# Optimization experiments

Measured on AMD Instinct MI355X. Metric: run time of the kernel, lower is better.

## Reference

```python
import jax, jax.numpy as jnp
import numpy as np
import math

D = 256          # cubic grid size
THICKNESS = 20   # sponge thickness
DT = 0.001
N_PML = 2
R_PML = 0.001


def _build_sigma(vmax, shape, thickness):
    # vectorized equivalent of the torch slab-assignment loop:
    # final value at a point is damping(min distance to any face) if < thickness else 0
    sigma0 = -(N_PML + 1) * vmax * math.log(R_PML) / (2.0 * thickness)
    dists = []
    for ax, n in enumerate(shape):
        idx = jnp.arange(n)
        d = jnp.minimum(idx, n - 1 - idx)
        sh = [1, 1, 1]
        sh[ax] = n
        dists.append(d.reshape(sh))
    mind = jnp.minimum(jnp.minimum(
        jnp.broadcast_to(dists[0], shape),
        jnp.broadcast_to(dists[1], shape)),
        jnp.broadcast_to(dists[2], shape)).astype(jnp.float32)
    damping = sigma0 * (1.0 - mind / thickness) ** N_PML
    return jnp.where(mind < thickness, damping, 0.0).astype(jnp.float32)


def setup_inputs() -> dict:
    key = jax.random.key(0)
    k1, k2, k3, k4 = jax.random.split(key, 4)
    shape = (D, D, D)
    source_cur = jax.random.normal(k1, shape, dtype=jnp.float32)
    p_cur = jax.random.normal(k2, shape, dtype=jnp.float32)
    p_pre = jax.random.normal(k3, shape, dtype=jnp.float32)
    v = 1500.0 + 1000.0 * jax.random.uniform(k4, shape, dtype=jnp.float32)
    a = v * v * (DT * DT)                      # v**2 * dt**2
    sigma = _build_sigma(float(jnp.max(v)), shape, THICKNESS)
    return {"source_cur": source_cur, "p_cur": p_cur, "p_pre": p_pre,
            "a": a, "sigma": sigma, "dt": DT}


def _laplacian7(p):
    # 7-point stencil with zero padding (matches conv3d(kernel, padding=1))
    pp = jnp.pad(p, 1)
    return (pp[2:, 1:-1, 1:-1] + pp[:-2, 1:-1, 1:-1]
            + pp[1:-1, 2:, 1:-1] + pp[1:-1, :-2, 1:-1]
            + pp[1:-1, 1:-1, 2:] + pp[1:-1, 1:-1, :-2]
            - 6.0 * p)


def reference(source_cur, p_cur, p_pre, a, sigma, dt):
    p_cur = p_cur + source_cur
    lap = _laplacian7(p_cur)
    half = 0.5 * sigma * dt
    p_new = (2.0 * p_cur - (1.0 - half) * p_pre + a * lap) / (1.0 + half)
    return (p_new, p_cur)
```

## Files before the change

kernel.cpp:

```cpp
#include <hip/hip_runtime.h>

#define DD 256
#define DD2 (DD * DD)
#define DD3 (DD * DD * DD)
#define TH 20

typedef float f32x4 __attribute__((ext_vector_type(4)));

__device__ __forceinline__ f32x4 ld4_sum(const float* __restrict__ p,
                                         const float* __restrict__ s,
                                         int idx) {
    return *reinterpret_cast<const f32x4*>(p + idx) +
           *reinterpret_cast<const f32x4*>(s + idx);
}

__device__ __forceinline__ f32x4 rcp4(f32x4 x) {
    f32x4 r;
    r.x = __builtin_amdgcn_rcpf(x.x);
    r.y = __builtin_amdgcn_rcpf(x.y);
    r.z = __builtin_amdgcn_rcpf(x.z);
    r.w = __builtin_amdgcn_rcpf(x.w);
    return r;
}

__global__ __launch_bounds__(256) void sponge_kernel(
    const float* __restrict__ src,
    const float* __restrict__ pc,
    const float* __restrict__ pp,
    const float* __restrict__ aa,
    const float* __restrict__ sg,
    const float* __restrict__ dtp,
    float* __restrict__ out_pnew,
    float* __restrict__ out_pcur)
{
    const float dt = dtp[0];

    const int lane = threadIdx.x & 63;
    const int w    = threadIdx.x >> 6;

    const int wid   = (blockIdx.x & 7) * 512 + (blockIdx.x >> 3);
    const int ytile = wid & 15;
    const int x     = wid >> 4;
    const int y0    = ytile * 16 + w * 4;
    const int basex = x * DD2 + lane * 4;

    f32x4 p4v[4], a4v[4];
#pragma unroll
    for (int r = 0; r < 4; ++r) {
        const int idx = basex + (y0 + r) * DD;
        p4v[r] = __builtin_nontemporal_load(reinterpret_cast<const f32x4*>(pp + idx));
        a4v[r] = __builtin_nontemporal_load(reinterpret_cast<const f32x4*>(aa + idx));
    }

    const bool xsp = (x < TH) | (x >= DD - TH);
    const bool zsp = (lane < TH / 4) | (lane >= (DD - TH + 3) / 4);
    f32x4 s4v[4];
#pragma unroll
    for (int r = 0; r < 4; ++r) {
        const int yy = y0 + r;
        const bool sp = xsp | zsp | (yy < TH) | (yy >= DD - TH);
        s4v[r] = sp ? *reinterpret_cast<const f32x4*>(sg + basex + yy * DD)
                    : (f32x4)(0.0f);
    }

    f32x4 uu[6];
#pragma unroll
    for (int r = 0; r < 6; ++r) {
        const int yy = y0 - 1 + r;
        uu[r] = (f32x4)(0.0f);
        if (yy >= 0 && yy < DD) uu[r] = ld4_sum(pc, src, basex + yy * DD);
    }

    f32x4 uxm[4], uxp[4];
#pragma unroll
    for (int r = 0; r < 4; ++r) {
        const int idx = basex + (y0 + r) * DD;
        uxm[r] = (f32x4)(0.0f);
        uxp[r] = (f32x4)(0.0f);
        if (x > 0)      uxm[r] = ld4_sum(pc, src, idx - DD2);
        if (x < DD - 1) uxp[r] = ld4_sum(pc, src, idx + DD2);
    }

#pragma unroll
    for (int r = 0; r < 4; ++r) {
        const int idx = basex + (y0 + r) * DD;
        const f32x4 u = uu[r + 1];

        float left  = __shfl_up(u.w, 1);
        float right = __shfl_down(u.x, 1);
        if (lane == 0)  left  = 0.0f;
        if (lane == 63) right = 0.0f;

        f32x4 lap;
        lap.x = left + u.y + uu[r].x + uu[r + 2].x + uxm[r].x + uxp[r].x - 6.0f * u.x;
        lap.y = u.x  + u.z + uu[r].y + uu[r + 2].y + uxm[r].y + uxp[r].y - 6.0f * u.y;
        lap.z = u.y  + u.w + uu[r].z + uu[r + 2].z + uxm[r].z + uxp[r].z - 6.0f * u.z;
        lap.w = u.z  + right + uu[r].w + uu[r + 2].w + uxm[r].w + uxp[r].w - 6.0f * u.w;

        const f32x4 half = (0.5f * dt) * s4v[r];
        const f32x4 num  = 2.0f * u - (1.0f - half) * p4v[r] + a4v[r] * lap;
        const f32x4 pn   = num * rcp4(1.0f + half);

        __builtin_nontemporal_store(pn, reinterpret_cast<f32x4*>(out_pnew + idx));
        __builtin_nontemporal_store(u,  reinterpret_cast<f32x4*>(out_pcur + idx));
    }
}

extern "C" void kernel_launch(void* const* d_in, const int* in_sizes, int n_in,
                              void* d_out, int out_size, void* d_ws, size_t ws_size,
                              hipStream_t stream) {
    const float* src = (const float*)d_in[0];
    const float* pc  = (const float*)d_in[1];
    const float* pp  = (const float*)d_in[2];
    const float* aa  = (const float*)d_in[3];
    const float* sg  = (const float*)d_in[4];
    const float* dtp = (const float*)d_in[5];
    float* out = (float*)d_out;

    const int grid = 16 * DD;
    sponge_kernel<<<grid, 256, 0, stream>>>(src, pc, pp, aa, sg, dtp,
                                            out, out + DD3);
}
```

Before: 79.07 us.

## March each wave through 8 x-planes with rolling register planes

Each wave now walks 8 consecutive x-planes and keeps three rolling register planes (x-1, x, x+1) of p_cur+source. This replaces the earlier scheme where every x-plane reloaded its x-1 and x+1 neighbours, cutting redundant global and L2 reads of the two summed input arrays. The grid shrinks by a factor of 8, to 512 blocks, and register pressure grows. That lowers parallelism and may hurt the ability to hide memory latency on a bandwidth-bound kernel.

```diff
diff --git a/kernel.cpp b/kernel.cpp
--- a/kernel.cpp
+++ b/kernel.cpp
@@ -4,6 +4,7 @@
 #define DD2 (DD * DD)
 #define DD3 (DD * DD * DD)
 #define TH 20
+#define XSEG 8
 
 typedef float f32x4 __attribute__((ext_vector_type(4)));
 
@@ -38,71 +39,88 @@
     const int lane = threadIdx.x & 63;
     const int w    = threadIdx.x >> 6;
 
-    const int wid   = (blockIdx.x & 7) * 512 + (blockIdx.x >> 3);
+    const int wid   = (blockIdx.x & 7) * 64 + (blockIdx.x >> 3);
     const int ytile = wid & 15;
-    const int x     = wid >> 4;
+    const int xseg  = wid >> 4;
     const int y0    = ytile * 16 + w * 4;
-    const int basex = x * DD2 + lane * 4;
+    const int x0    = xseg * XSEG;
+    const int basez = lane * 4;
 
-    f32x4 p4v[4], a4v[4];
-#pragma unroll
-    for (int r = 0; r < 4; ++r) {
-        const int idx = basex + (y0 + r) * DD;
-        p4v[r] = __builtin_nontemporal_load(reinterpret_cast<const f32x4*>(pp + idx));
-        a4v[r] = __builtin_nontemporal_load(reinterpret_cast<const f32x4*>(aa + idx));
-    }
+    const bool zsp = (lane < TH / 4) | (lane >= (DD - TH + 3) / 4);
 
-    const bool xsp = (x < TH) | (x >= DD - TH);
-    const bool zsp = (lane < TH / 4) | (lane >= (DD - TH + 3) / 4);
-    f32x4 s4v[4];
-#pragma unroll
-    for (int r = 0; r < 4; ++r) {
-        const int yy = y0 + r;
-        const bool sp = xsp | zsp | (yy < TH) | (yy >= DD - TH);
-        s4v[r] = sp ? *reinterpret_cast<const f32x4*>(sg + basex + yy * DD)
-                    : (f32x4)(0.0f);
-    }
+    f32x4 colA[6], colB[6], colC[6];
 
-    f32x4 uu[6];
 #pragma unroll
     for (int r = 0; r < 6; ++r) {
         const int yy = y0 - 1 + r;
-        uu[r] = (f32x4)(0.0f);
-        if (yy >= 0 && yy < DD) uu[r] = ld4_sum(pc, src, basex + yy * DD);
-    }
-
-    f32x4 uxm[4], uxp[4];
-#pragma unroll
-    for (int r = 0; r < 4; ++r) {
-        const int idx = basex + (y0 + r) * DD;
-        uxm[r] = (f32x4)(0.0f);
-        uxp[r] = (f32x4)(0.0f);
-        if (x > 0)      uxm[r] = ld4_sum(pc, src, idx - DD2);
-        if (x < DD - 1) uxp[r] = ld4_sum(pc, src, idx + DD2);
+        colA[r] = (f32x4)(0.0f);
+        colB[r] = (f32x4)(0.0f);
+        if (yy >= 0 && yy < DD) {
+            if (x0 > 0) colA[r] = ld4_sum(pc, src, (x0 - 1) * DD2 + yy * DD + basez);
+            colB[r] = ld4_sum(pc, src, x0 * DD2 + yy * DD + basez);
+        }
     }
 
 #pragma unroll
-    for (int r = 0; r < 4; ++r) {
-        const int idx = basex + (y0 + r) * DD;
-        const f32x4 u = uu[r + 1];
+    for (int st = 0; st < XSEG; ++st) {
+        const int x  = x0 + st;
+        const int pb = x * DD2 + basez;
 
-        float left  = __shfl_up(u.w, 1);
-        float right = __shfl_down(u.x, 1);
-        if (lane == 0)  left  = 0.0f;
-        if (lane == 63) right = 0.0f;
+        f32x4 p4v[4], a4v[4];
+#pragma unroll
+        for (int r = 0; r < 4; ++r) {
+            const int idx = pb + (y0 + r) * DD;
+            p4v[r] = __builtin_nontemporal_load(reinterpret_cast<const f32x4*>(pp + idx));
+            a4v[r] = __builtin_nontemporal_load(reinterpret_cast<const f32x4*>(aa + idx));
+        }
 
-        f32x4 lap;
-        lap.x = left + u.y + uu[r].x + uu[r + 2].x + uxm[r].x + uxp[r].x - 6.0f * u.x;
-        lap.y = u.x  + u.z + uu[r].y + uu[r + 2].y + uxm[r].y + uxp[r].y - 6.0f * u.y;
-        lap.z = u.y  + u.w + uu[r].z + uu[r + 2].z + uxm[r].z + uxp[r].z - 6.0f * u.z;
-        lap.w = u.z  + right + uu[r].w + uu[r + 2].w + uxm[r].w + uxp[r].w - 6.0f * u.w;
+        const bool xsp = (x < TH) | (x >= DD - TH);
+        f32x4 s4v[4];
+#pragma unroll
+        for (int r = 0; r < 4; ++r) {
+            const int yy = y0 + r;
+            const bool sp = xsp | zsp | (yy < TH) | (yy >= DD - TH);
+            s4v[r] = sp ? *reinterpret_cast<const f32x4*>(sg + pb + yy * DD)
+                        : (f32x4)(0.0f);
+        }
 
-        const f32x4 half = (0.5f * dt) * s4v[r];
-        const f32x4 num  = 2.0f * u - (1.0f - half) * p4v[r] + a4v[r] * lap;
-        const f32x4 pn   = num * rcp4(1.0f + half);
+#pragma unroll
+        for (int r = 0; r < 6; ++r) {
+            const int yy = y0 - 1 + r;
+            colC[r] = (f32x4)(0.0f);
+            if (x < DD - 1 && yy >= 0 && yy < DD)
+                colC[r] = ld4_sum(pc, src, (x + 1) * DD2 + yy * DD + basez);
+        }
 
-        __builtin_nontemporal_store(pn, reinterpret_cast<f32x4*>(out_pnew + idx));
-        __builtin_nontemporal_store(u,  reinterpret_cast<f32x4*>(out_pcur + idx));
+#pragma unroll
+        for (int r = 0; r < 4; ++r) {
+            const int idx = pb + (y0 + r) * DD;
+            const f32x4 u = colB[r + 1];
+
+            float left  = __shfl_up(u.w, 1);
+            float right = __shfl_down(u.x, 1);
+            if (lane == 0)  left  = 0.0f;
+            if (lane == 63) right = 0.0f;
+
+            f32x4 lap;
+            lap.x = left  + u.y + colB[r].x + colB[r + 2].x + colA[r + 1].x + colC[r + 1].x - 6.0f * u.x;
+            lap.y = u.x   + u.z + colB[r].y + colB[r + 2].y + colA[r + 1].y + colC[r + 1].y - 6.0f * u.y;
+            lap.z = u.y   + u.w + colB[r].z + colB[r + 2].z + colA[r + 1].z + colC[r + 1].z - 6.0f * u.z;
+            lap.w = u.z   + right + colB[r].w + colB[r + 2].w + colA[r + 1].w + colC[r + 1].w - 6.0f * u.w;
+
+            const f32x4 half = (0.5f * dt) * s4v[r];
+            const f32x4 num  = 2.0f * u - (1.0f - half) * p4v[r] + a4v[r] * lap;
+            const f32x4 pn   = num * rcp4(1.0f + half);
+
+            __builtin_nontemporal_store(pn, reinterpret_cast<f32x4*>(out_pnew + idx));
+            __builtin_nontemporal_store(u,  reinterpret_cast<f32x4*>(out_pcur + idx));
+        }
+
+#pragma unroll
+        for (int r = 0; r < 6; ++r) {
+            colA[r] = colB[r];
+            colB[r] = colC[r];
+        }
     }
 }
 
@@ -117,7 +135,7 @@
     const float* dtp = (const float*)d_in[5];
     float* out = (float*)d_out;
 
-    const int grid = 16 * DD;
+    const int grid = 16 * (DD / XSEG);
     sponge_kernel<<<grid, 256, 0, stream>>>(src, pc, pp, aa, sg, dtp,
                                             out, out + DD3);
 }
```

Result: slower. 85.73 us (+8.4%).
